# Optimization experiments

Measured on AMD Instinct MI355X. Metric: run time of the kernel, lower is better.

## Reference

```python
import jax, jax.numpy as jnp
import numpy as np
import math

B, S, HID = 2, 2048, 1024
D = 64            # size_per_head
H = HID // D      # num heads = 16
ROT = 32          # rotary_hsize = size_per_head // 2


def _apply_rotary(qk, sinusoids):
    # qk: [B, S, H, D]; sinusoids: [B, 2, S, ROT]
    sin = sinusoids[:, 0, :, None, :]   # [B, S, 1, ROT]
    cos = sinusoids[:, 1, :, None, :]
    qk_rope = qk[..., :ROT]
    # torch.stack([-a[..., ::2], a[..., 1::2]], -1).reshape(a.shape)
    rot2 = jnp.stack([-qk_rope[..., ::2], qk_rope[..., 1::2]], axis=-1).reshape(qk_rope.shape)
    qk_rope = qk_rope * cos + rot2 * sin
    return jnp.concatenate([qk_rope, qk[..., ROT:]], axis=-1)


def setup_inputs() -> dict:
    key = jax.random.key(0)
    ks = jax.random.split(key, 8)
    sc = 1.0 / math.sqrt(HID)
    return {
        "x": jax.random.normal(ks[0], (B, S, HID), jnp.float32),
        "sinusoids": jax.random.normal(ks[1], (B, 2, S, ROT), jnp.float32),
        "attention_bias": jax.random.uniform(ks[2], (B, 1, S, S), jnp.float32),
        "Wq": jax.random.normal(ks[3], (HID, HID), jnp.float32) * sc,
        "bq": jnp.zeros((HID,), jnp.float32),
        "Wk": jax.random.normal(ks[4], (HID, HID), jnp.float32) * sc,
        "bk": jnp.zeros((HID,), jnp.float32),
        "Wv": jax.random.normal(ks[5], (HID, HID), jnp.float32) * sc,
        "bv": jnp.zeros((HID,), jnp.float32),
        "Wo": jax.random.normal(ks[6], (HID, HID), jnp.float32) * sc,
    }


def reference(x, sinusoids, attention_bias, Wq, bq, Wk, bk, Wv, bv, Wo):
    q = (x @ Wq + bq).reshape(B, S, H, D)
    k = (x @ Wk + bk).reshape(B, S, H, D)
    v = (x @ Wv + bv).reshape(B, S, H, D)
    # original concatenates q,k along the heads dim before rotary; since rotary
    # broadcasts over heads, applying it to each separately is identical math
    q = _apply_rotary(q, sinusoids)
    k = _apply_rotary(k, sinusoids)
    q = q / math.sqrt(D)
    scores = jnp.einsum('bqhd,bkhd->bhqk', q, k)          # [B,H,S,S]
    probs = jax.nn.softmax(scores, axis=-1)
    probs = probs * attention_bias                         # multiplicative bias AFTER softmax
    out = jnp.einsum('bhqk,bkhd->bqhd', probs, v)          # [B,S,H,D]
    out = out.reshape(B, S, HID)
    return out @ Wo
```

## Files before the change

### kernel.cpp

```cpp
#include <hip/hip_runtime.h>
#include <hip/hip_bf16.h>
#include <math.h>

#define B_   2
#define S_   2048
#define HID_ 1024
#define D_   64
#define H_   16
#define ROT_ 32
#define M_   (B_*S_)
#define NSPLIT 2
#define KSPAN (S_ / NSPLIT)
#define NT    (KSPAN / 64)

typedef __attribute__((ext_vector_type(4))) short  short4v;
typedef __attribute__((ext_vector_type(8))) short  short8;
typedef __attribute__((ext_vector_type(4))) float  floatx4;
typedef __attribute__((ext_vector_type(16))) float floatx16;

__device__ __forceinline__ float bf2f(unsigned short u) {
  unsigned int x = ((unsigned int)u) << 16;
  return __builtin_bit_cast(float, x);
}
__device__ __forceinline__ unsigned short f2bf(float f) {
  unsigned int x = __builtin_bit_cast(unsigned int, f);
  x += 0x7fffu + ((x >> 16) & 1u);
  return (unsigned short)(x >> 16);
}
__device__ __forceinline__ unsigned int pkbf(float a, float b) {
  __hip_bfloat162 h = __float22bfloat162_rn(float2{a, b});
  unsigned int u; __builtin_memcpy(&u, &h, 4); return u;
}
__device__ __forceinline__ void gload_lds16(const unsigned short* g, unsigned short* l) {
  __builtin_amdgcn_global_load_lds(
      (const __attribute__((address_space(1))) unsigned int*)g,
      (__attribute__((address_space(3))) unsigned int*)l, 16, 0, 0);
}

__global__ void cast_bf16(const float* __restrict__ in, unsigned short* __restrict__ out) {
  int i = (blockIdx.x * 256 + threadIdx.x) * 4;
  floatx4 v = *(const floatx4*)(in + i);
  unsigned short o[4];
  o[0] = f2bf(v[0]); o[1] = f2bf(v[1]); o[2] = f2bf(v[2]); o[3] = f2bf(v[3]);
  *(unsigned long long*)(out + i) = *(unsigned long long*)o;
}

__global__ void transW(const float* __restrict__ W0, const float* __restrict__ W1,
                       const float* __restrict__ W2, const float* __restrict__ W3,
                       unsigned short* __restrict__ T0, unsigned short* __restrict__ T1,
                       unsigned short* __restrict__ T2, unsigned short* __restrict__ T3) {
  const float* W; unsigned short* T;
  int z = blockIdx.z;
  if (z == 0)      { W = W0; T = T0; }
  else if (z == 1) { W = W1; T = T1; }
  else if (z == 2) { W = W2; T = T2; }
  else             { W = W3; T = T3; }
  __shared__ float tile[32][33];
  int bx = blockIdx.x * 32, by = blockIdx.y * 32;
  int tx = threadIdx.x, ty = threadIdx.y;
  #pragma unroll
  for (int j = 0; j < 4; j++)
    tile[ty + j*8][tx] = W[(size_t)(by + ty + j*8) * HID_ + bx + tx];
  __syncthreads();
  #pragma unroll
  for (int j = 0; j < 4; j++)
    T[(size_t)(bx + ty + j*8) * HID_ + by + tx] = f2bf(tile[tx][ty + j*8]);
}

template <int MODE>
__global__ __launch_bounds__(256) void gemm_bt(
    const unsigned short* __restrict__ A,
    const unsigned short* __restrict__ Bt0, const unsigned short* __restrict__ Bt1,
    const unsigned short* __restrict__ Bt2,
    const float* __restrict__ bias0, const float* __restrict__ bias1,
    const float* __restrict__ bias2,
    void* __restrict__ out0, void* __restrict__ out1, void* __restrict__ out2,
    const float* __restrict__ sins, float sc0)
{
  const unsigned short* Bt; const float* bias; void* Out; float sc;
  if (blockIdx.z == 0)      { Bt = Bt0; bias = bias0; Out = out0; sc = sc0; }
  else if (blockIdx.z == 1) { Bt = Bt1; bias = bias1; Out = out1; sc = 1.f; }
  else                      { Bt = Bt2; bias = bias2; Out = out2; sc = 1.f; }
  const int K = HID_, N = HID_;
  int m0 = blockIdx.y * 128, n0 = blockIdx.x * 128;
  __shared__ alignas(16) unsigned short sA[128 * 32];
  __shared__ alignas(16) unsigned short sB[128 * 32];
  int t = threadIdx.x;
  int lane = t & 63, wave = t >> 6;
  int quad = lane >> 4, l16 = lane & 15;
  int wr = wave >> 1, wc = wave & 1;

  int srow = (lane >> 2), scol = (lane & 3) * 8;
  const unsigned short* gA0 = A  + (size_t)(m0 + wave*32 +  0 + srow) * K + scol;
  const unsigned short* gA1 = A  + (size_t)(m0 + wave*32 + 16 + srow) * K + scol;
  const unsigned short* gB0 = Bt + (size_t)(n0 + wave*32 +  0 + srow) * K + scol;
  const unsigned short* gB1 = Bt + (size_t)(n0 + wave*32 + 16 + srow) * K + scol;
  unsigned short* lA0 = sA + (wave*32 +  0) * 32;
  unsigned short* lA1 = sA + (wave*32 + 16) * 32;
  unsigned short* lB0 = sB + (wave*32 +  0) * 32;
  unsigned short* lB1 = sB + (wave*32 + 16) * 32;

  floatx4 acc[4][4];
  #pragma unroll
  for (int i = 0; i < 4; i++)
    #pragma unroll
    for (int j = 0; j < 4; j++)
      acc[i][j] = (floatx4){0.f, 0.f, 0.f, 0.f};

  for (int k0 = 0; k0 < K; k0 += 32) {
    gload_lds16(gA0 + k0, lA0);
    gload_lds16(gA1 + k0, lA1);
    gload_lds16(gB0 + k0, lB0);
    gload_lds16(gB1 + k0, lB1);
    __syncthreads();
    short8 af[4], bf[4];
    #pragma unroll
    for (int i = 0; i < 4; i++) {
      af[i] = *(const short8*)(sA + (wr * 64 + i * 16 + l16) * 32 + quad * 8);
      bf[i] = *(const short8*)(sB + (wc * 64 + i * 16 + l16) * 32 + quad * 8);
    }
    #pragma unroll
    for (int i = 0; i < 4; i++)
      #pragma unroll
      for (int j = 0; j < 4; j++)
        acc[i][j] = __builtin_amdgcn_mfma_f32_16x16x32_bf16(af[i], bf[j], acc[i][j], 0, 0, 0);
    __syncthreads();
  }

  #pragma unroll
  for (int i = 0; i < 4; i++) {
    int mbase = m0 + wr * 64 + i * 16 + quad * 4;
    #pragma unroll
    for (int j = 0; j < 4; j++) {
      int n = n0 + wc * 64 + j * 16 + l16;
      float bv = bias ? bias[n] : 0.f;
      if (MODE == 1) {
        #pragma unroll
        for (int r = 0; r < 4; r++)
          ((float*)Out)[(size_t)(mbase + r) * N + n] = acc[i][j][r] + bv;
      } else if (blockIdx.z == 2) {
        int bb = mbase >> 11, ss = mbase & 2047;
        int hh = n >> 6, dd = n & 63;
        unsigned short pk[4];
        #pragma unroll
        for (int r = 0; r < 4; r++) pk[r] = f2bf(acc[i][j][r] + bv);
        *(unsigned long long*)((unsigned short*)Out +
            (((size_t)(bb * H_ + hh) * D_ + dd) * S_ + ss)) = *(unsigned long long*)pk;
      } else if (j < 2) {
        int jh = j * 16 + l16;
        #pragma unroll
        for (int r = 0; r < 4; r++) {
          int row = mbase + r, bb = row >> 11, ss = row & 2047;
          float sn = sins[((size_t)(bb * 2 + 0) * S_ + ss) * ROT_ + jh];
          float cs = sins[((size_t)(bb * 2 + 1) * S_ + ss) * ROT_ + jh];
          float f = (jh & 1) ? (cs + sn) : (cs - sn);
          ((unsigned short*)Out)[(size_t)row * N + n] = f2bf((acc[i][j][r] + bv) * f * sc);
        }
      } else {
        #pragma unroll
        for (int r = 0; r < 4; r++)
          ((unsigned short*)Out)[(size_t)(mbase + r) * N + n] = f2bf((acc[i][j][r] + bv) * sc);
      }
    }
  }
}

__global__ __launch_bounds__(256) void attn(
    const unsigned short* __restrict__ Q, const unsigned short* __restrict__ Kb,
    const unsigned short* __restrict__ Vt, const float* __restrict__ bias,
    float* __restrict__ Opart, float* __restrict__ Lpart)
{
  int gid = blockIdx.x;
  int c = gid & 7, h = (gid >> 3) & 15, g = gid >> 7;
  int combo = g * 8 + c;
  int qtile = combo & 15;
  int rest  = combo >> 4;
  int b = rest & 1, split = rest >> 1;

  int t = threadIdx.x;
  int lane = t & 63, wave = t >> 6;
  int l32 = lane & 31, hl = lane >> 5;
  int q0 = qtile * 128 + wave * 32;
  int kbase = split * KSPAN;
  const int RS = H_ * D_;
  const size_t pidx = ((size_t)(b * NSPLIT + split) * H_ + h) * (S_ / 128) + qtile;
  float* Oslab = Opart + pidx * (128 * 64);
  float* Lslab = Lpart + pidx * 128;

  __shared__ alignas(16) unsigned short sK[2][64 * 72];
  __shared__ alignas(16) unsigned short sV[2][64 * 72];

  const unsigned short* Qbase = Q + ((size_t)(b * S_) * H_ + h) * D_;
  const unsigned short* Kbase = Kb + ((size_t)(b * S_ + kbase) * H_ + h) * D_;
  const unsigned short* Vbase = Vt + (((size_t)(b * H_) + h) * D_) * S_ + kbase;

  short8 qf[4];
  {
    const unsigned short* qp = Qbase + (size_t)(q0 + l32) * RS + 8 * hl;
    qf[0] = *(const short8*)(qp);
    qf[1] = *(const short8*)(qp + 16);
    qf[2] = *(const short8*)(qp + 32);
    qf[3] = *(const short8*)(qp + 48);
  }

  int srow = t >> 2, sq = t & 3;
  const unsigned short* gK = Kbase + (size_t)srow * RS + sq * 16;
  const unsigned short* gV = Vbase + (size_t)srow * S_ + sq * 16;
  const int wOff = srow * 72 + sq * 16;

  const float* bp = bias + (size_t)b * S_ * S_ + (size_t)(q0 + l32) * S_ + kbase + 4 * hl;

  float l_run = 0.f;
  floatx16 o0, o1;
  #pragma unroll
  for (int r = 0; r < 16; r++) { o0[r] = 0.f; o1[r] = 0.f; }

  floatx4 kp[2], vp[2];
  kp[0] = *(const floatx4*)(gK);     kp[1] = *(const floatx4*)(gK + 8);
  vp[0] = *(const floatx4*)(gV);     vp[1] = *(const floatx4*)(gV + 8);
  *(floatx4*)(&sK[0][wOff])     = kp[0];
  *(floatx4*)(&sK[0][wOff + 8]) = kp[1];
  *(floatx4*)(&sV[0][wOff])     = vp[0];
  *(floatx4*)(&sV[0][wOff + 8]) = vp[1];
  kp[0] = *(const floatx4*)(gK + (size_t)64 * RS);
  kp[1] = *(const floatx4*)(gK + (size_t)64 * RS + 8);
  vp[0] = *(const floatx4*)(gV + 64);
  vp[1] = *(const floatx4*)(gV + 64 + 8);

  for (int it = 0; it < NT; ++it) {
    int cur = it & 1, nxt = cur ^ 1;
    int kt = it * 64;
    __syncthreads();

    if (it < NT - 1) {
      *(floatx4*)(&sK[nxt][wOff])     = kp[0];
      *(floatx4*)(&sK[nxt][wOff + 8]) = kp[1];
      *(floatx4*)(&sV[nxt][wOff])     = vp[0];
      *(floatx4*)(&sV[nxt][wOff + 8]) = vp[1];
    }
    {
      int k2 = ((it + 2) & (NT - 1)) * 64;
      kp[0] = *(const floatx4*)(gK + (size_t)k2 * RS);
      kp[1] = *(const floatx4*)(gK + (size_t)k2 * RS + 8);
      vp[0] = *(const floatx4*)(gV + k2);
      vp[1] = *(const floatx4*)(gV + k2 + 8);
    }

    floatx4 bl[8];
    #pragma unroll
    for (int cc = 0; cc < 2; cc++)
      #pragma unroll
      for (int rg = 0; rg < 4; rg++)
        bl[cc * 4 + rg] = *(const floatx4*)(bp + kt + cc * 32 + 8 * rg);

    floatx16 st[2];
    #pragma unroll
    for (int cc = 0; cc < 2; cc++) {
      floatx16 s;
      #pragma unroll
      for (int r = 0; r < 16; r++) s[r] = 0.f;
      #pragma unroll
      for (int ks = 0; ks < 4; ks++) {
        short8 kf = *(const short8*)(&sK[cur][(cc * 32 + l32) * 72 + 16 * ks + 8 * hl]);
        s = __builtin_amdgcn_mfma_f32_32x32x16_bf16(kf, qf[ks], s, 0, 0, 0);
      }
      st[cc] = s;
    }

    short4v pf[2][4];
    #pragma unroll
    for (int cc = 0; cc < 2; cc++)
      #pragma unroll
      for (int rg = 0; rg < 4; rg++) {
        float p0 = __builtin_amdgcn_exp2f(st[cc][rg * 4 + 0]);
        float p1 = __builtin_amdgcn_exp2f(st[cc][rg * 4 + 1]);
        float p2 = __builtin_amdgcn_exp2f(st[cc][rg * 4 + 2]);
        float p3 = __builtin_amdgcn_exp2f(st[cc][rg * 4 + 3]);
        l_run += (p0 + p1) + (p2 + p3);
        floatx4 bv = bl[cc * 4 + rg];
        unsigned int lo = pkbf(p0 * bv[0], p1 * bv[1]);
        unsigned int hi = pkbf(p2 * bv[2], p3 * bv[3]);
        union { unsigned int u[2]; short4v s4; } u;
        u.u[0] = lo; u.u[1] = hi;
        pf[cc][rg] = u.s4;
      }

    #pragma unroll
    for (int cc = 0; cc < 2; cc++)
      #pragma unroll
      for (int g2 = 0; g2 < 4; g2++) {
        int kcol = cc * 32 + 8 * g2 + 4 * hl;
        short4v vf0 = *(const short4v*)(&sV[cur][(l32)      * 72 + kcol]);
        short4v vf1 = *(const short4v*)(&sV[cur][(32 + l32) * 72 + kcol]);
        o0 = __builtin_amdgcn_mfma_f32_32x32x8bf16_1k(pf[cc][g2], vf0, o0, 0, 0, 0);
        o1 = __builtin_amdgcn_mfma_f32_32x32x8bf16_1k(pf[cc][g2], vf1, o1, 0, 0, 0);
      }
  }

  float lsum = l_run + __shfl_xor(l_run, 32);
  if (hl == 0) Lslab[wave * 32 + l32] = lsum;
  #pragma unroll
  for (int r = 0; r < 16; r++) {
    int q_local = wave * 32 + (r & 3) + 8 * (r >> 2) + 4 * hl;
    Oslab[(size_t)q_local * 64 + l32]      = o0[r];
    Oslab[(size_t)q_local * 64 + 32 + l32] = o1[r];
  }
}

__global__ __launch_bounds__(256) void combine(
    const float* __restrict__ Opart, const float* __restrict__ Lpart,
    unsigned short* __restrict__ Ab)
{
  int qt = blockIdx.x, h = blockIdx.y, b = blockIdx.z;
  int t = threadIdx.x;
  int q = t >> 1, d0 = (t & 1) * 32;
  size_t p0 = ((size_t)(b * NSPLIT + 0) * H_ + h) * (S_ / 128) + qt;
  size_t p1 = ((size_t)(b * NSPLIT + 1) * H_ + h) * (S_ / 128) + qt;
  float linv = __builtin_amdgcn_rcpf(Lpart[p0 * 128 + q] + Lpart[p1 * 128 + q]);
  const float* O0 = Opart + p0 * (128 * 64) + (size_t)q * 64 + d0;
  const float* O1 = Opart + p1 * (128 * 64) + (size_t)q * 64 + d0;
  unsigned short* dst = Ab + ((size_t)(b * S_ + qt * 128 + q) * H_ + h) * D_ + d0;
  #pragma unroll
  for (int i = 0; i < 8; i++) {
    floatx4 a = *(const floatx4*)(O0 + 4 * i);
    floatx4 c = *(const floatx4*)(O1 + 4 * i);
    a = a + c;
    unsigned int w[2];
    w[0] = pkbf(a[0] * linv, a[1] * linv);
    w[1] = pkbf(a[2] * linv, a[3] * linv);
    *(unsigned long long*)(dst + 4 * i) = *(unsigned long long*)w;
  }
}

extern "C" void kernel_launch(void* const* d_in, const int* in_sizes, int n_in,
                              void* d_out, int out_size, void* d_ws, size_t ws_size,
                              hipStream_t stream) {
  (void)in_sizes; (void)n_in; (void)out_size; (void)ws_size;
  const float* x    = (const float*)d_in[0];
  const float* sins = (const float*)d_in[1];
  const float* ab   = (const float*)d_in[2];
  const float* Wq   = (const float*)d_in[3];
  const float* bq   = (const float*)d_in[4];
  const float* Wk   = (const float*)d_in[5];
  const float* bk   = (const float*)d_in[6];
  const float* Wv   = (const float*)d_in[7];
  const float* bv   = (const float*)d_in[8];
  const float* Wo   = (const float*)d_in[9];
  float* out = (float*)d_out;
  char* ws = (char*)d_ws;

  unsigned short* xb  = (unsigned short*)(ws);
  unsigned short* Wqt = (unsigned short*)(ws + ((size_t) 8 << 20));
  unsigned short* Wkt = (unsigned short*)(ws + ((size_t)10 << 20));
  unsigned short* Wvt = (unsigned short*)(ws + ((size_t)12 << 20));
  unsigned short* Wot = (unsigned short*)(ws + ((size_t)14 << 20));
  unsigned short* Qb  = (unsigned short*)(ws + ((size_t)16 << 20));
  unsigned short* Kb  = (unsigned short*)(ws + ((size_t)24 << 20));
  unsigned short* Vtb = (unsigned short*)(ws + ((size_t)32 << 20));
  unsigned short* Ab  = (unsigned short*)(ws + ((size_t)40 << 20));
  float*          Opart = (float*)(ws + ((size_t)48 << 20));
  float*          Lpart = (float*)(ws + ((size_t)80 << 20));

  const float c1 = 0.125f * 1.44269504088896f;

  cast_bf16<<<dim3((M_ * HID_) / (256 * 4)), dim3(256), 0, stream>>>(x, xb);
  transW<<<dim3(32, 32, 4), dim3(32, 8), 0, stream>>>(Wq, Wk, Wv, Wo, Wqt, Wkt, Wvt, Wot);
  gemm_bt<0><<<dim3(8, 32, 3), dim3(256), 0, stream>>>(xb, Wqt, Wkt, Wvt, bq, bk, bv,
                                                       Qb, Kb, Vtb, sins, c1);
  attn<<<dim3((S_ / 128) * H_ * B_ * NSPLIT), dim3(256), 0, stream>>>(Qb, Kb, Vtb, ab,
                                                                      Opart, Lpart);
  combine<<<dim3(S_ / 128, H_, B_), dim3(256), 0, stream>>>(Opart, Lpart, Ab);
  gemm_bt<1><<<dim3(8, 32, 1), dim3(256), 0, stream>>>(Ab, Wot, Wot, Wot,
                                                       nullptr, nullptr, nullptr,
                                                       out, out, out, sins, 1.f);
}
```

Baseline: 285.8 us.

## Process two heads per attention block to reuse bias tile loads

Each attention workgroup now handles a pair of heads for the same query tile and key split, so the fp32 attention bias tile loaded from global memory serves both heads instead of being re-read per head. The grid shrinks to half as many blocks, and LDS doubles to hold K/V tiles for both heads. This cuts the dominant bias bandwidth (bias is shared across heads), at the cost of higher register pressure (two sets of Q fragments and output accumulators) and fewer, larger blocks, which may lower occupancy.

```diff
diff --git a/kernel.cpp b/kernel.cpp
--- a/kernel.cpp
+++ b/kernel.cpp
@@ -171,11 +171,10 @@
     float* __restrict__ Opart, float* __restrict__ Lpart)
 {
   int gid = blockIdx.x;
-  int c = gid & 7, h = (gid >> 3) & 15, g = gid >> 7;
-  int combo = g * 8 + c;
+  int hp = gid >> 6;
+  int combo = gid & 63;
   int qtile = combo & 15;
-  int rest  = combo >> 4;
-  int b = rest & 1, split = rest >> 1;
+  int b = (combo >> 4) & 1, split = combo >> 5;
 
   int t = threadIdx.x;
   int lane = t & 63, wave = t >> 6;
@@ -183,49 +182,59 @@
   int q0 = qtile * 128 + wave * 32;
   int kbase = split * KSPAN;
   const int RS = H_ * D_;
-  const size_t pidx = ((size_t)(b * NSPLIT + split) * H_ + h) * (S_ / 128) + qtile;
-  float* Oslab = Opart + pidx * (128 * 64);
-  float* Lslab = Lpart + pidx * 128;
-
-  __shared__ alignas(16) unsigned short sK[2][64 * 72];
-  __shared__ alignas(16) unsigned short sV[2][64 * 72];
-
-  const unsigned short* Qbase = Q + ((size_t)(b * S_) * H_ + h) * D_;
-  const unsigned short* Kbase = Kb + ((size_t)(b * S_ + kbase) * H_ + h) * D_;
-  const unsigned short* Vbase = Vt + (((size_t)(b * H_) + h) * D_) * S_ + kbase;
-
-  short8 qf[4];
-  {
-    const unsigned short* qp = Qbase + (size_t)(q0 + l32) * RS + 8 * hl;
-    qf[0] = *(const short8*)(qp);
-    qf[1] = *(const short8*)(qp + 16);
-    qf[2] = *(const short8*)(qp + 32);
-    qf[3] = *(const short8*)(qp + 48);
+
+  __shared__ alignas(16) unsigned short sK[2][2][64 * 72];
+  __shared__ alignas(16) unsigned short sV[2][2][64 * 72];
+
+  const unsigned short* Qb0 = Q + ((size_t)(b * S_) * H_ + hp * 2) * D_;
+  const unsigned short* Kb0 = Kb + ((size_t)(b * S_ + kbase) * H_ + hp * 2) * D_;
+  const unsigned short* Vb0 = Vt + (((size_t)(b * H_) + hp * 2) * D_) * S_ + kbase;
+
+  short8 qf[2][4];
+  #pragma unroll
+  for (int hh = 0; hh < 2; hh++) {
+    const unsigned short* qp = Qb0 + (size_t)hh * D_ + (size_t)(q0 + l32) * RS + 8 * hl;
+    qf[hh][0] = *(const short8*)(qp);
+    qf[hh][1] = *(const short8*)(qp + 16);
+    qf[hh][2] = *(const short8*)(qp + 32);
+    qf[hh][3] = *(const short8*)(qp + 48);
   }
 
   int srow = t >> 2, sq = t & 3;
-  const unsigned short* gK = Kbase + (size_t)srow * RS + sq * 16;
-  const unsigned short* gV = Vbase + (size_t)srow * S_ + sq * 16;
+  const unsigned short* gK[2]; const unsigned short* gV[2];
+  #pragma unroll
+  for (int hh = 0; hh < 2; hh++) {
+    gK[hh] = Kb0 + (size_t)srow * RS + (size_t)hh * D_ + sq * 16;
+    gV[hh] = Vb0 + ((size_t)hh * D_ + srow) * S_ + sq * 16;
+  }
   const int wOff = srow * 72 + sq * 16;
 
   const float* bp = bias + (size_t)b * S_ * S_ + (size_t)(q0 + l32) * S_ + kbase + 4 * hl;
 
-  float l_run = 0.f;
-  floatx16 o0, o1;
-  #pragma unroll
-  for (int r = 0; r < 16; r++) { o0[r] = 0.f; o1[r] = 0.f; }
-
-  floatx4 kp[2], vp[2];
-  kp[0] = *(const floatx4*)(gK);     kp[1] = *(const floatx4*)(gK + 8);
-  vp[0] = *(const floatx4*)(gV);     vp[1] = *(const floatx4*)(gV + 8);
-  *(floatx4*)(&sK[0][wOff])     = kp[0];
-  *(floatx4*)(&sK[0][wOff + 8]) = kp[1];
-  *(floatx4*)(&sV[0][wOff])     = vp[0];
-  *(floatx4*)(&sV[0][wOff + 8]) = vp[1];
-  kp[0] = *(const floatx4*)(gK + (size_t)64 * RS);
-  kp[1] = *(const floatx4*)(gK + (size_t)64 * RS + 8);
-  vp[0] = *(const floatx4*)(gV + 64);
-  vp[1] = *(const floatx4*)(gV + 64 + 8);
+  float l_run[2] = {0.f, 0.f};
+  floatx16 oacc[2][2];
+  #pragma unroll
+  for (int hh = 0; hh < 2; hh++)
+    #pragma unroll
+    for (int r = 0; r < 16; r++) { oacc[hh][0][r] = 0.f; oacc[hh][1][r] = 0.f; }
+
+  floatx4 kp[2][2], vp[2][2];
+  #pragma unroll
+  for (int hh = 0; hh < 2; hh++) {
+    kp[hh][0] = *(const floatx4*)(gK[hh]);  kp[hh][1] = *(const floatx4*)(gK[hh] + 8);
+    vp[hh][0] = *(const floatx4*)(gV[hh]);  vp[hh][1] = *(const floatx4*)(gV[hh] + 8);
+    *(floatx4*)(&sK[0][hh][wOff])     = kp[hh][0];
+    *(floatx4*)(&sK[0][hh][wOff + 8]) = kp[hh][1];
+    *(floatx4*)(&sV[0][hh][wOff])     = vp[hh][0];
+    *(floatx4*)(&sV[0][hh][wOff + 8]) = vp[hh][1];
+  }
+  #pragma unroll
+  for (int hh = 0; hh < 2; hh++) {
+    kp[hh][0] = *(const floatx4*)(gK[hh] + (size_t)64 * RS);
+    kp[hh][1] = *(const floatx4*)(gK[hh] + (size_t)64 * RS + 8);
+    vp[hh][0] = *(const floatx4*)(gV[hh] + 64);
+    vp[hh][1] = *(const floatx4*)(gV[hh] + 64 + 8);
+  }
 
   for (int it = 0; it < NT; ++it) {
     int cur = it & 1, nxt = cur ^ 1;
@@ -233,17 +242,23 @@
     __syncthreads();
 
     if (it < NT - 1) {
-      *(floatx4*)(&sK[nxt][wOff])     = kp[0];
-      *(floatx4*)(&sK[nxt][wOff + 8]) = kp[1];
-      *(floatx4*)(&sV[nxt][wOff])     = vp[0];
-      *(floatx4*)(&sV[nxt][wOff + 8]) = vp[1];
+      #pragma unroll
+      for (int hh = 0; hh < 2; hh++) {
+        *(floatx4*)(&sK[nxt][hh][wOff])     = kp[hh][0];
+        *(floatx4*)(&sK[nxt][hh][wOff + 8]) = kp[hh][1];
+        *(floatx4*)(&sV[nxt][hh][wOff])     = vp[hh][0];
+        *(floatx4*)(&sV[nxt][hh][wOff + 8]) = vp[hh][1];
+      }
     }
     {
       int k2 = ((it + 2) & (NT - 1)) * 64;
-      kp[0] = *(const floatx4*)(gK + (size_t)k2 * RS);
-      kp[1] = *(const floatx4*)(gK + (size_t)k2 * RS + 8);
-      vp[0] = *(const floatx4*)(gV + k2);
-      vp[1] = *(const floatx4*)(gV + k2 + 8);
+      #pragma unroll
+      for (int hh = 0; hh < 2; hh++) {
+        kp[hh][0] = *(const floatx4*)(gK[hh] + (size_t)(k2) * RS);
+        kp[hh][1] = *(const floatx4*)(gK[hh] + (size_t)(k2) * RS + 8);
+        vp[hh][0] = *(const floatx4*)(gV[hh] + k2);
+        vp[hh][1] = *(const floatx4*)(gV[hh] + k2 + 8);
+      }
     }
 
     floatx4 bl[8];
@@ -253,57 +268,67 @@
       for (int rg = 0; rg < 4; rg++)
         bl[cc * 4 + rg] = *(const floatx4*)(bp + kt + cc * 32 + 8 * rg);
 
-    floatx16 st[2];
-    #pragma unroll
-    for (int cc = 0; cc < 2; cc++) {
-      floatx16 s;
-      #pragma unroll
-      for (int r = 0; r < 16; r++) s[r] = 0.f;
-      #pragma unroll
-      for (int ks = 0; ks < 4; ks++) {
-        short8 kf = *(const short8*)(&sK[cur][(cc * 32 + l32) * 72 + 16 * ks + 8 * hl]);
-        s = __builtin_amdgcn_mfma_f32_32x32x16_bf16(kf, qf[ks], s, 0, 0, 0);
+    #pragma unroll
+    for (int hh = 0; hh < 2; hh++) {
+      floatx16 st[2];
+      #pragma unroll
+      for (int cc = 0; cc < 2; cc++) {
+        floatx16 s;
+        #pragma unroll
+        for (int r = 0; r < 16; r++) s[r] = 0.f;
+        #pragma unroll
+        for (int ks = 0; ks < 4; ks++) {
+          short8 kf = *(const short8*)(&sK[cur][hh][(cc * 32 + l32) * 72 + 16 * ks + 8 * hl]);
+          s = __builtin_amdgcn_mfma_f32_32x32x16_bf16(kf, qf[hh][ks], s, 0, 0, 0);
+        }
+        st[cc] = s;
       }
-      st[cc] = s;
-    }
-
-    short4v pf[2][4];
-    #pragma unroll
-    for (int cc = 0; cc < 2; cc++)
-      #pragma unroll
-      for (int rg = 0; rg < 4; rg++) {
-        float p0 = __builtin_amdgcn_exp2f(st[cc][rg * 4 + 0]);
-        float p1 = __builtin_amdgcn_exp2f(st[cc][rg * 4 + 1]);
-        float p2 = __builtin_amdgcn_exp2f(st[cc][rg * 4 + 2]);
-        float p3 = __builtin_amdgcn_exp2f(st[cc][rg * 4 + 3]);
-        l_run += (p0 + p1) + (p2 + p3);
-        floatx4 bv = bl[cc * 4 + rg];
-        unsigned int lo = pkbf(p0 * bv[0], p1 * bv[1]);
-        unsigned int hi = pkbf(p2 * bv[2], p3 * bv[3]);
-        union { unsigned int u[2]; short4v s4; } u;
-        u.u[0] = lo; u.u[1] = hi;
-        pf[cc][rg] = u.s4;
-      }
-
-    #pragma unroll
-    for (int cc = 0; cc < 2; cc++)
-      #pragma unroll
-      for (int g2 = 0; g2 < 4; g2++) {
-        int kcol = cc * 32 + 8 * g2 + 4 * hl;
-        short4v vf0 = *(const short4v*)(&sV[cur][(l32)      * 72 + kcol]);
-        short4v vf1 = *(const short4v*)(&sV[cur][(32 + l32) * 72 + kcol]);
-        o0 = __builtin_amdgcn_mfma_f32_32x32x8bf16_1k(pf[cc][g2], vf0, o0, 0, 0, 0);
-        o1 = __builtin_amdgcn_mfma_f32_32x32x8bf16_1k(pf[cc][g2], vf1, o1, 0, 0, 0);
-      }
-  }
-
-  float lsum = l_run + __shfl_xor(l_run, 32);
-  if (hl == 0) Lslab[wave * 32 + l32] = lsum;
-  #pragma unroll
-  for (int r = 0; r < 16; r++) {
-    int q_local = wave * 32 + (r & 3) + 8 * (r >> 2) + 4 * hl;
-    Oslab[(size_t)q_local * 64 + l32]      = o0[r];
-    Oslab[(size_t)q_local * 64 + 32 + l32] = o1[r];
+
+      short4v pf[2][4];
+      #pragma unroll
+      for (int cc = 0; cc < 2; cc++)
+        #pragma unroll
+        for (int rg = 0; rg < 4; rg++) {
+          float p0 = __builtin_amdgcn_exp2f(st[cc][rg * 4 + 0]);
+          float p1 = __builtin_amdgcn_exp2f(st[cc][rg * 4 + 1]);
+          float p2 = __builtin_amdgcn_exp2f(st[cc][rg * 4 + 2]);
+          float p3 = __builtin_amdgcn_exp2f(st[cc][rg * 4 + 3]);
+          l_run[hh] += (p0 + p1) + (p2 + p3);
+          floatx4 bv = bl[cc * 4 + rg];
+          unsigned int lo = pkbf(p0 * bv[0], p1 * bv[1]);
+          unsigned int hi = pkbf(p2 * bv[2], p3 * bv[3]);
+          union { unsigned int u[2]; short4v s4; } u;
+          u.u[0] = lo; u.u[1] = hi;
+          pf[cc][rg] = u.s4;
+        }
+
+      #pragma unroll
+      for (int cc = 0; cc < 2; cc++)
+        #pragma unroll
+        for (int g2 = 0; g2 < 4; g2++) {
+          int kcol = cc * 32 + 8 * g2 + 4 * hl;
+          short4v vf0 = *(const short4v*)(&sV[cur][hh][(l32)      * 72 + kcol]);
+          short4v vf1 = *(const short4v*)(&sV[cur][hh][(32 + l32) * 72 + kcol]);
+          oacc[hh][0] = __builtin_amdgcn_mfma_f32_32x32x8bf16_1k(pf[cc][g2], vf0, oacc[hh][0], 0, 0, 0);
+          oacc[hh][1] = __builtin_amdgcn_mfma_f32_32x32x8bf16_1k(pf[cc][g2], vf1, oacc[hh][1], 0, 0, 0);
+        }
+    }
+  }
+
+  #pragma unroll
+  for (int hh = 0; hh < 2; hh++) {
+    int h = hp * 2 + hh;
+    const size_t pidx = ((size_t)(b * NSPLIT + split) * H_ + h) * (S_ / 128) + qtile;
+    float* Oslab = Opart + pidx * (128 * 64);
+    float* Lslab = Lpart + pidx * 128;
+    float lsum = l_run[hh] + __shfl_xor(l_run[hh], 32);
+    if (hl == 0) Lslab[wave * 32 + l32] = lsum;
+    #pragma unroll
+    for (int r = 0; r < 16; r++) {
+      int q_local = wave * 32 + (r & 3) + 8 * (r >> 2) + 4 * hl;
+      Oslab[(size_t)q_local * 64 + l32]      = oacc[hh][0][r];
+      Oslab[(size_t)q_local * 64 + 32 + l32] = oacc[hh][1][r];
+    }
   }
 }
 
@@ -367,8 +392,7 @@
   transW<<<dim3(32, 32, 4), dim3(32, 8), 0, stream>>>(Wq, Wk, Wv, Wo, Wqt, Wkt, Wvt, Wot);
   gemm_bt<0><<<dim3(8, 32, 3), dim3(256), 0, stream>>>(xb, Wqt, Wkt, Wvt, bq, bk, bv,
                                                        Qb, Kb, Vtb, sins, c1);
-  attn<<<dim3((S_ / 128) * H_ * B_ * NSPLIT), dim3(256), 0, stream>>>(Qb, Kb, Vtb, ab,
-                                                                      Opart, Lpart);
+  attn<<<dim3((H_ / 2) * 64), dim3(256), 0, stream>>>(Qb, Kb, Vtb, ab, Opart, Lpart);
   combine<<<dim3(S_ / 128, H_, B_), dim3(256), 0, stream>>>(Opart, Lpart, Ab);
   gemm_bt<1><<<dim3(8, 32, 1), dim3(256), 0, stream>>>(Ab, Wot, Wot, Wot,
                                                        nullptr, nullptr, nullptr,
```

Result: slower. 307.3 us (+7.6%).

## Pre-swizzle bias to bf16 fragment layout and store Q/K/V head-major tiles

Applied to the files above, without the earlier changes.

Adds a prepass kernel that converts the fp32 attention bias into bf16, laid out in the exact per-lane fragment order the attention loop consumes. The attention kernel then reads the bias as contiguous 8-byte chunks, not strided fp32 rows. The QKV GEMM epilogue now writes Q and K head-major ([B,H,S,D]) and V as 64-wide tiles, so K/V tile loads become contiguous. This halves the bias bytes read inside attention and gives coalesced K/V/Q loads. In exchange it adds a separate full pass over the 32MB fp32 bias and rounds the bias to bf16.

```diff
diff --git a/kernel.cpp b/kernel.cpp
--- a/kernel.cpp
+++ b/kernel.cpp
@@ -65,6 +65,23 @@
   #pragma unroll
   for (int j = 0; j < 4; j++)
     T[(size_t)(bx + ty + j*8) * HID_ + by + tx] = f2bf(tile[tx][ty + j*8]);
+}
+
+__global__ __launch_bounds__(256) void prepB(const float* __restrict__ bias,
+                                             unsigned short* __restrict__ out) {
+  int qb = blockIdx.x, kb = blockIdx.y, b = blockIdx.z;
+  int t = threadIdx.x;
+  int l32 = t & 31, g = t >> 5;
+  int cc = g >> 2, rg = g & 3;
+  const float* src = bias + ((size_t)b * S_ + qb * 32 + l32) * S_ + kb * 64 + cc * 32 + rg * 8;
+  unsigned short* dst = out + ((((size_t)(b * 64 + qb)) * 32 + kb) * 8 + g) * 256 + l32 * 4;
+  floatx4 v0 = *(const floatx4*)(src);
+  floatx4 v1 = *(const floatx4*)(src + 4);
+  unsigned int w0[2], w1[2];
+  w0[0] = pkbf(v0[0], v0[1]); w0[1] = pkbf(v0[2], v0[3]);
+  w1[0] = pkbf(v1[0], v1[1]); w1[1] = pkbf(v1[2], v1[3]);
+  *(unsigned long long*)(dst)       = *(unsigned long long*)w0;
+  *(unsigned long long*)(dst + 128) = *(unsigned long long*)w1;
 }
 
 template <int MODE>
@@ -144,30 +161,36 @@
         unsigned short pk[4];
         #pragma unroll
         for (int r = 0; r < 4; r++) pk[r] = f2bf(acc[i][j][r] + bv);
-        *(unsigned long long*)((unsigned short*)Out +
-            (((size_t)(bb * H_ + hh) * D_ + dd) * S_ + ss)) = *(unsigned long long*)pk;
+        size_t idx = ((((size_t)(bb * H_ + hh) * (S_ / 64) + (ss >> 6)) * D_ + dd) * 64) + (ss & 63);
+        *(unsigned long long*)((unsigned short*)Out + idx) = *(unsigned long long*)pk;
       } else if (j < 2) {
         int jh = j * 16 + l16;
+        int hh = n >> 6, dd = n & 63;
         #pragma unroll
         for (int r = 0; r < 4; r++) {
           int row = mbase + r, bb = row >> 11, ss = row & 2047;
           float sn = sins[((size_t)(bb * 2 + 0) * S_ + ss) * ROT_ + jh];
           float cs = sins[((size_t)(bb * 2 + 1) * S_ + ss) * ROT_ + jh];
           float f = (jh & 1) ? (cs + sn) : (cs - sn);
-          ((unsigned short*)Out)[(size_t)row * N + n] = f2bf((acc[i][j][r] + bv) * f * sc);
+          ((unsigned short*)Out)[((size_t)(bb * H_ + hh) * S_ + ss) * D_ + dd] =
+              f2bf((acc[i][j][r] + bv) * f * sc);
         }
       } else {
+        int hh = n >> 6, dd = n & 63;
         #pragma unroll
-        for (int r = 0; r < 4; r++)
-          ((unsigned short*)Out)[(size_t)(mbase + r) * N + n] = f2bf((acc[i][j][r] + bv) * sc);
+        for (int r = 0; r < 4; r++) {
+          int row = mbase + r, bb = row >> 11, ss = row & 2047;
+          ((unsigned short*)Out)[((size_t)(bb * H_ + hh) * S_ + ss) * D_ + dd] =
+              f2bf((acc[i][j][r] + bv) * sc);
+        }
       }
     }
   }
 }
 
 __global__ __launch_bounds__(256) void attn(
-    const unsigned short* __restrict__ Q, const unsigned short* __restrict__ Kb,
-    const unsigned short* __restrict__ Vt, const float* __restrict__ bias,
+    const unsigned short* __restrict__ Q, const unsigned short* __restrict__ Kh,
+    const unsigned short* __restrict__ Vt, const unsigned short* __restrict__ Bsw,
     float* __restrict__ Opart, float* __restrict__ Lpart)
 {
   int gid = blockIdx.x;
@@ -182,7 +205,6 @@
   int l32 = lane & 31, hl = lane >> 5;
   int q0 = qtile * 128 + wave * 32;
   int kbase = split * KSPAN;
-  const int RS = H_ * D_;
   const size_t pidx = ((size_t)(b * NSPLIT + split) * H_ + h) * (S_ / 128) + qtile;
   float* Oslab = Opart + pidx * (128 * 64);
   float* Lslab = Lpart + pidx * 128;
@@ -190,13 +212,15 @@
   __shared__ alignas(16) unsigned short sK[2][64 * 72];
   __shared__ alignas(16) unsigned short sV[2][64 * 72];
 
-  const unsigned short* Qbase = Q + ((size_t)(b * S_) * H_ + h) * D_;
-  const unsigned short* Kbase = Kb + ((size_t)(b * S_ + kbase) * H_ + h) * D_;
-  const unsigned short* Vbase = Vt + (((size_t)(b * H_) + h) * D_) * S_ + kbase;
+  const unsigned short* Qbase = Q + ((size_t)(b * H_ + h) * S_) * D_;
+  const unsigned short* gK0 = Kh + ((size_t)(b * H_ + h) * S_ + kbase) * D_ + t * 16;
+  const unsigned short* gV0 = Vt + (((size_t)(b * H_ + h) * (S_ / 64) + split * NT) * D_) * 64 + t * 16;
+  const unsigned short* bt0 = Bsw +
+      (((size_t)(b * 64 + (q0 >> 5)) * 32 + split * NT) * 8) * 256 + hl * 128 + l32 * 4;
 
   short8 qf[4];
   {
-    const unsigned short* qp = Qbase + (size_t)(q0 + l32) * RS + 8 * hl;
+    const unsigned short* qp = Qbase + (size_t)(q0 + l32) * D_ + 8 * hl;
     qf[0] = *(const short8*)(qp);
     qf[1] = *(const short8*)(qp + 16);
     qf[2] = *(const short8*)(qp + 32);
@@ -204,11 +228,7 @@
   }
 
   int srow = t >> 2, sq = t & 3;
-  const unsigned short* gK = Kbase + (size_t)srow * RS + sq * 16;
-  const unsigned short* gV = Vbase + (size_t)srow * S_ + sq * 16;
   const int wOff = srow * 72 + sq * 16;
-
-  const float* bp = bias + (size_t)b * S_ * S_ + (size_t)(q0 + l32) * S_ + kbase + 4 * hl;
 
   float l_run = 0.f;
   floatx16 o0, o1;
@@ -216,20 +236,19 @@
   for (int r = 0; r < 16; r++) { o0[r] = 0.f; o1[r] = 0.f; }
 
   floatx4 kp[2], vp[2];
-  kp[0] = *(const floatx4*)(gK);     kp[1] = *(const floatx4*)(gK + 8);
-  vp[0] = *(const floatx4*)(gV);     vp[1] = *(const floatx4*)(gV + 8);
+  kp[0] = *(const floatx4*)(gK0);     kp[1] = *(const floatx4*)(gK0 + 8);
+  vp[0] = *(const floatx4*)(gV0);     vp[1] = *(const floatx4*)(gV0 + 8);
   *(floatx4*)(&sK[0][wOff])     = kp[0];
   *(floatx4*)(&sK[0][wOff + 8]) = kp[1];
   *(floatx4*)(&sV[0][wOff])     = vp[0];
   *(floatx4*)(&sV[0][wOff + 8]) = vp[1];
-  kp[0] = *(const floatx4*)(gK + (size_t)64 * RS);
-  kp[1] = *(const floatx4*)(gK + (size_t)64 * RS + 8);
-  vp[0] = *(const floatx4*)(gV + 64);
-  vp[1] = *(const floatx4*)(gV + 64 + 8);
+  kp[0] = *(const floatx4*)(gK0 + 4096);
+  kp[1] = *(const floatx4*)(gK0 + 4096 + 8);
+  vp[0] = *(const floatx4*)(gV0 + 4096);
+  vp[1] = *(const floatx4*)(gV0 + 4096 + 8);
 
   for (int it = 0; it < NT; ++it) {
     int cur = it & 1, nxt = cur ^ 1;
-    int kt = it * 64;
     __syncthreads();
 
     if (it < NT - 1) {
@@ -239,19 +258,20 @@
       *(floatx4*)(&sV[nxt][wOff + 8]) = vp[1];
     }
     {
-      int k2 = ((it + 2) & (NT - 1)) * 64;
-      kp[0] = *(const floatx4*)(gK + (size_t)k2 * RS);
-      kp[1] = *(const floatx4*)(gK + (size_t)k2 * RS + 8);
-      vp[0] = *(const floatx4*)(gV + k2);
-      vp[1] = *(const floatx4*)(gV + k2 + 8);
-    }
-
-    floatx4 bl[8];
-    #pragma unroll
-    for (int cc = 0; cc < 2; cc++)
-      #pragma unroll
-      for (int rg = 0; rg < 4; rg++)
-        bl[cc * 4 + rg] = *(const floatx4*)(bp + kt + cc * 32 + 8 * rg);
+      size_t o = (size_t)(((it + 2) & (NT - 1))) * 4096;
+      kp[0] = *(const floatx4*)(gK0 + o);
+      kp[1] = *(const floatx4*)(gK0 + o + 8);
+      vp[0] = *(const floatx4*)(gV0 + o);
+      vp[1] = *(const floatx4*)(gV0 + o + 8);
+    }
+
+    unsigned long long braw[8];
+    {
+      const unsigned short* bt = bt0 + (size_t)it * 2048;
+      #pragma unroll
+      for (int gg = 0; gg < 8; gg++)
+        braw[gg] = *(const unsigned long long*)(bt + gg * 256);
+    }
 
     floatx16 st[2];
     #pragma unroll
@@ -277,12 +297,16 @@
         float p2 = __builtin_amdgcn_exp2f(st[cc][rg * 4 + 2]);
         float p3 = __builtin_amdgcn_exp2f(st[cc][rg * 4 + 3]);
         l_run += (p0 + p1) + (p2 + p3);
-        floatx4 bv = bl[cc * 4 + rg];
-        unsigned int lo = pkbf(p0 * bv[0], p1 * bv[1]);
-        unsigned int hi = pkbf(p2 * bv[2], p3 * bv[3]);
-        union { unsigned int u[2]; short4v s4; } u;
-        u.u[0] = lo; u.u[1] = hi;
-        pf[cc][rg] = u.s4;
+        unsigned long long u = braw[cc * 4 + rg];
+        float b0 = bf2f((unsigned short)(u));
+        float b1 = bf2f((unsigned short)(u >> 16));
+        float b2 = bf2f((unsigned short)(u >> 32));
+        float b3 = bf2f((unsigned short)(u >> 48));
+        unsigned int lo = pkbf(p0 * b0, p1 * b1);
+        unsigned int hi = pkbf(p2 * b2, p3 * b3);
+        union { unsigned int w[2]; short4v s4; } uu;
+        uu.w[0] = lo; uu.w[1] = hi;
+        pf[cc][rg] = uu.s4;
       }
 
     #pragma unroll
@@ -358,16 +382,18 @@
   unsigned short* Kb  = (unsigned short*)(ws + ((size_t)24 << 20));
   unsigned short* Vtb = (unsigned short*)(ws + ((size_t)32 << 20));
   unsigned short* Ab  = (unsigned short*)(ws + ((size_t)40 << 20));
-  float*          Opart = (float*)(ws + ((size_t)48 << 20));
-  float*          Lpart = (float*)(ws + ((size_t)80 << 20));
+  unsigned short* Bsw = (unsigned short*)(ws + ((size_t)48 << 20));
+  float*          Opart = (float*)(ws + ((size_t)65 << 20));
+  float*          Lpart = (float*)(ws + ((size_t)97 << 20));
 
   const float c1 = 0.125f * 1.44269504088896f;
 
+  prepB<<<dim3(64, 32, 2), dim3(256), 0, stream>>>(ab, Bsw);
   cast_bf16<<<dim3((M_ * HID_) / (256 * 4)), dim3(256), 0, stream>>>(x, xb);
   transW<<<dim3(32, 32, 4), dim3(32, 8), 0, stream>>>(Wq, Wk, Wv, Wo, Wqt, Wkt, Wvt, Wot);
   gemm_bt<0><<<dim3(8, 32, 3), dim3(256), 0, stream>>>(xb, Wqt, Wkt, Wvt, bq, bk, bv,
                                                        Qb, Kb, Vtb, sins, c1);
-  attn<<<dim3((S_ / 128) * H_ * B_ * NSPLIT), dim3(256), 0, stream>>>(Qb, Kb, Vtb, ab,
+  attn<<<dim3((S_ / 128) * H_ * B_ * NSPLIT), dim3(256), 0, stream>>>(Qb, Kb, Vtb, Bsw,
                                                                       Opart, Lpart);
   combine<<<dim3(S_ / 128, H_, B_), dim3(256), 0, stream>>>(Opart, Lpart, Ab);
   gemm_bt<1><<<dim3(8, 32, 1), dim3(256), 0, stream>>>(Ab, Wot, Wot, Wot,
```

New measurement: 283.7 us. No clear change (-0.7%).
